# Optimization experiments

Measured on AMD Instinct MI355X. Metric: run time of the kernel, lower is better.

## Reference

```python
import jax, jax.numpy as jnp
import numpy as np

N_NODES = 20000
DEG = 16
T_IN = 12
T_OUT = 24
N_HEADS = 4
N_CH = 4
BATCH = 2


def setup_inputs() -> dict:
    key = jax.random.key(0)
    k1, k2, k3, k4 = jax.random.split(key, 4)
    # unique directed edges: (i, (i+d) % N) for d in 1..DEG, plus self loops
    src = jnp.repeat(jnp.arange(N_NODES, dtype=jnp.int64), DEG)
    offs = jnp.tile(jnp.arange(1, DEG + 1, dtype=jnp.int64), N_NODES)
    dst = (src + offs) % N_NODES
    loops = jnp.arange(N_NODES, dtype=jnp.int64)
    d_edges = jnp.concatenate([
        jnp.stack([src, dst], axis=1),
        jnp.stack([loops, loops], axis=1),
    ], axis=0)  # (E, 2), E = N*DEG + N
    E = d_edges.shape[0]
    x = jax.random.normal(k1, (BATCH, T_IN, N_NODES, N_CH), dtype=jnp.float32)
    d_ew = jax.random.uniform(k2, (E, N_HEADS), dtype=jnp.float32)
    # shrink: Linear(t_in*n_heads -> T-t_in)
    fan_in = T_IN * N_HEADS
    bound = 1.0 / np.sqrt(fan_in)
    W = jax.random.uniform(k3, (T_OUT - T_IN, fan_in), minval=-bound, maxval=bound, dtype=jnp.float32)
    b = jax.random.uniform(k4, (T_OUT - T_IN,), minval=-bound, maxval=bound, dtype=jnp.float32)
    return {"x": x, "d_ew": d_ew, "W": W, "b": b, "d_edges": d_edges}


def reference(x, d_ew, W, b, d_edges):
    # x: (B, t, N, C); d_ew: (E, H); d_edges: (E, 2)
    node_i = d_edges[:, 0]
    node_j = d_edges[:, 1]
    B, t, N, C = x.shape
    # gather source node features per edge -> (E, B, t, C)
    x_src = jnp.moveaxis(x[:, :, node_i, :], 2, 0)
    # messages: (E, B, t, H, C)
    msg = d_ew[:, None, None, :, None] * x_src[:, :, :, None, :]
    # scatter-add into destination nodes (equivalent to the dense N x N holder sum)
    agg = jax.ops.segment_sum(msg, node_j, num_segments=N)  # (N, B, t, H, C)
    y = jnp.moveaxis(agg, 0, 2)                              # (B, t, N, H, C)
    # permute(0,2,4,1,3) -> (B, N, C, t, H), flatten (t, H)
    y = jnp.transpose(y, (0, 2, 4, 1, 3)).reshape(B, N, C, t * d_ew.shape[1])
    y = jax.nn.relu(jnp.einsum('bncf,of->bnco', y, W) + b)   # (B, N, C, T-t)
    y = jnp.transpose(y, (0, 3, 1, 2))                       # (B, T-t, N, C)
    return jnp.concatenate([x, y], axis=1)                   # (B, T, N, C)
```

## Files before the change

kernel.cpp:

```cpp
#include <hip/hip_runtime.h>

namespace {
constexpr int NN  = 20000;
constexpr int DEG = 16;
constexpr int TI  = 12;
constexpr int TO  = 24;
constexpr int NC  = 4;
constexpr int NB  = 2;
constexpr int ESELF  = NN * DEG;
constexpr int TILE   = 32;
constexpr int NTILES = NN / TILE;
constexpr int WN     = TILE + 16;
constexpr int EWP    = 68;
}

__global__ __launch_bounds__(256) void gnn_fused(
    const float* __restrict__ x,
    const float* __restrict__ ew,
    const float* __restrict__ W,
    const float* __restrict__ bias,
    float* __restrict__ out)
{
    __shared__ float x_lds[TI * WN * NC];
    __shared__ float ew_lds[WN * EWP];
    __shared__ float ews[TILE * 4];
    __shared__ float red[TILE * NC][13];

    const int tid = threadIdx.x;
    const int bid = blockIdx.x;
    const int b   = bid / NTILES;
    const int n0  = (bid % NTILES) * TILE;

    const float4* ew4 = reinterpret_cast<const float4*>(ew);

#pragma unroll
    for (int i = 0; i < 3; ++i) {
        const int idx = tid + 256 * i;
        const int sl  = idx >> 4;
        const int r4  = idx & 15;
        int s = n0 - 16 + sl;
        s += (s >> 31) & NN;
        const float4 v = ew4[s * DEG + r4];
        *reinterpret_cast<float4*>(&ew_lds[sl * EWP + r4 * 4]) = v;
    }
    if (tid < TILE) {
        const float4 v = ew4[ESELF + n0 + tid];
        *reinterpret_cast<float4*>(&ews[tid * 4]) = v;
    }
    {
        const size_t xb = (size_t)b * TI * NN * NC;
#pragma unroll
        for (int i = 0; i < 9; ++i) {
            const int f = tid + 256 * i;
            const int t = f / (WN * NC);
            const int r = f - t * (WN * NC);
            int s = n0 - 16 + (r >> 2);
            s += (s >> 31) & NN;
            x_lds[f] = x[xb + (size_t)t * NN * NC + s * NC + (r & 3)];
        }
    }
    __syncthreads();

    const int tg = tid >> 7;
    const int nl = (tid >> 2) & 31;
    const int c  = tid & 3;
    const int t0 = __builtin_amdgcn_readfirstlane(tg * 6);

    float agg[6][4] = {{0.f}};

#pragma unroll
    for (int k = 0; k < DEG; ++k) {
        const int wi = nl + 15 - k;
        const float4 w = *reinterpret_cast<const float4*>(&ew_lds[wi * EWP + 4 * k]);
#pragma unroll
        for (int j = 0; j < 6; ++j) {
            const float xv = x_lds[(t0 + j) * (WN * NC) + wi * 4 + c];
            agg[j][0] = fmaf(w.x, xv, agg[j][0]);
            agg[j][1] = fmaf(w.y, xv, agg[j][1]);
            agg[j][2] = fmaf(w.z, xv, agg[j][2]);
            agg[j][3] = fmaf(w.w, xv, agg[j][3]);
        }
    }

    const size_t obase = (size_t)b * TO * NN * NC + (n0 + nl) * NC + c;

    {
        const float4 w = *reinterpret_cast<const float4*>(&ews[nl * 4]);
        const int wi = nl + 16;
#pragma unroll
        for (int j = 0; j < 6; ++j) {
            const float xv = x_lds[(t0 + j) * (WN * NC) + wi * 4 + c];
            out[obase + (size_t)(t0 + j) * NN * NC] = xv;
            agg[j][0] = fmaf(w.x, xv, agg[j][0]);
            agg[j][1] = fmaf(w.y, xv, agg[j][1]);
            agg[j][2] = fmaf(w.z, xv, agg[j][2]);
            agg[j][3] = fmaf(w.w, xv, agg[j][3]);
        }
    }

    float y[12];
#pragma unroll
    for (int o = 0; o < 12; ++o) {
        float acc = 0.f;
#pragma unroll
        for (int j = 0; j < 6; ++j)
#pragma unroll
            for (int h = 0; h < 4; ++h)
                acc = fmaf(W[o * 48 + (t0 + j) * 4 + h], agg[j][h], acc);
        y[o] = acc;
    }

    if (tg == 1) {
#pragma unroll
        for (int o = 0; o < 12; ++o) red[nl * 4 + c][o] = y[o];
    }
    __syncthreads();
    if (tg == 0) {
#pragma unroll
        for (int o = 0; o < 12; ++o) {
            const float v = fmaxf(y[o] + red[nl * 4 + c][o] + bias[o], 0.f);
            out[obase + (size_t)(TI + o) * NN * NC] = v;
        }
    }
}

extern "C" void kernel_launch(void* const* d_in, const int* in_sizes, int n_in,
                              void* d_out, int out_size, void* d_ws, size_t ws_size,
                              hipStream_t stream) {
    const float* x    = (const float*)d_in[0];
    const float* ew   = (const float*)d_in[1];
    const float* W    = (const float*)d_in[2];
    const float* bias = (const float*)d_in[3];
    float* out = (float*)d_out;

    const int blocks = NB * NTILES;
    hipLaunchKernelGGL(gnn_fused, dim3(blocks), dim3(256), 0, stream,
                       x, ew, W, bias, out);
}
```

Measured before the change: 16.98 us.

## Use packed FMA with two channels per thread and async global-to-LDS loads

Halves the block to 128 threads, with each thread handling two channels as float2 and updating them through v_pk_fma_f32 inline asm with op_sel broadcasts. The x tile is loaded by __builtin_amdgcn_global_load_lds, 16 bytes per lane, instead of per-float register staging. Outputs and the reduction buffer move to float2 stores. This aims to cut FMA issue count and load instructions, but it doubles per-thread register use and relies on correct handling of the LDS-direct layout and wait semantics.

```diff
diff --git a/kernel.cpp b/kernel.cpp
--- a/kernel.cpp
+++ b/kernel.cpp
@@ -4,122 +4,150 @@
 constexpr int NN  = 20000;
 constexpr int DEG = 16;
 constexpr int TI  = 12;
-constexpr int TO  = 24;
-constexpr int NC  = 4;
 constexpr int NB  = 2;
 constexpr int ESELF  = NN * DEG;
 constexpr int TILE   = 32;
 constexpr int NTILES = NN / TILE;
-constexpr int WN     = TILE + 16;
+constexpr int WN     = 48;
 constexpr int EWP    = 68;
+constexpr int REDP   = 13;
 }
 
-__global__ __launch_bounds__(256) void gnn_fused(
+__device__ __forceinline__ void pk_fma(float2& d, float2 a, float2 b) {
+    asm("v_pk_fma_f32 %0, %1, %2, %0" : "+v"(d) : "v"(a), "v"(b));
+}
+__device__ __forceinline__ void pk_fma_blo(float2& d, float2 a, float2 b) {
+    asm("v_pk_fma_f32 %0, %1, %2, %0 op_sel:[0,0,0] op_sel_hi:[1,0,1]"
+        : "+v"(d) : "v"(a), "v"(b));
+}
+__device__ __forceinline__ void pk_fma_bhi(float2& d, float2 a, float2 b) {
+    asm("v_pk_fma_f32 %0, %1, %2, %0 op_sel:[0,1,0] op_sel_hi:[1,1,1]"
+        : "+v"(d) : "v"(a), "v"(b));
+}
+
+__global__ __launch_bounds__(128) void gnn_fused(
     const float* __restrict__ x,
     const float* __restrict__ ew,
     const float* __restrict__ W,
     const float* __restrict__ bias,
     float* __restrict__ out)
 {
-    __shared__ float x_lds[TI * WN * NC];
+    __shared__ float x_lds[TI * WN * 4];
     __shared__ float ew_lds[WN * EWP];
     __shared__ float ews[TILE * 4];
-    __shared__ float red[TILE * NC][13];
+    __shared__ float red[TILE * 2 * REDP * 2];
 
     const int tid = threadIdx.x;
     const int bid = blockIdx.x;
     const int b   = bid / NTILES;
     const int n0  = (bid % NTILES) * TILE;
 
-    const float4* ew4 = reinterpret_cast<const float4*>(ew);
-
+    {
+        const float* xb = x + (size_t)b * TI * NN * 4;
 #pragma unroll
-    for (int i = 0; i < 3; ++i) {
-        const int idx = tid + 256 * i;
-        const int sl  = idx >> 4;
-        const int r4  = idx & 15;
-        int s = n0 - 16 + sl;
-        s += (s >> 31) & NN;
-        const float4 v = ew4[s * DEG + r4];
-        *reinterpret_cast<float4*>(&ew_lds[sl * EWP + r4 * 4]) = v;
-    }
-    if (tid < TILE) {
-        const float4 v = ew4[ESELF + n0 + tid];
-        *reinterpret_cast<float4*>(&ews[tid * 4]) = v;
+        for (int i = 0; i < 5; ++i) {
+            if (i < 4 || tid < 64) {
+                const int idx4 = tid + 128 * i;
+                const int t  = idx4 / WN;
+                const int wi = idx4 - t * WN;
+                int s = n0 - 16 + wi; s += (s >> 31) & NN;
+                const float* src = xb + (size_t)(t * NN + s) * 4;
+                float* dstbase = x_lds + (size_t)(128 * i + (tid & 64)) * 4;
+                __builtin_amdgcn_global_load_lds(
+                    (const __attribute__((address_space(1))) void*)src,
+                    (__attribute__((address_space(3))) void*)dstbase, 16, 0, 0);
+            }
+        }
     }
     {
-        const size_t xb = (size_t)b * TI * NN * NC;
+        const float4* ew4 = (const float4*)ew;
 #pragma unroll
-        for (int i = 0; i < 9; ++i) {
-            const int f = tid + 256 * i;
-            const int t = f / (WN * NC);
-            const int r = f - t * (WN * NC);
-            int s = n0 - 16 + (r >> 2);
-            s += (s >> 31) & NN;
-            x_lds[f] = x[xb + (size_t)t * NN * NC + s * NC + (r & 3)];
+        for (int i = 0; i < 6; ++i) {
+            const int idx = tid + 128 * i;
+            const int sl = idx >> 4, r4 = idx & 15;
+            int s = n0 - 16 + sl; s += (s >> 31) & NN;
+            const float4 v = ew4[s * DEG + r4];
+            *(float4*)&ew_lds[sl * EWP + r4 * 4] = v;
         }
+        if (tid < TILE) ((float4*)ews)[tid] = ew4[ESELF + n0 + tid];
     }
     __syncthreads();
 
-    const int tg = tid >> 7;
-    const int nl = (tid >> 2) & 31;
-    const int c  = tid & 3;
+    const int c2 = tid & 1;
+    const int nl = (tid >> 1) & 31;
+    const int tg = tid >> 6;
     const int t0 = __builtin_amdgcn_readfirstlane(tg * 6);
 
-    float agg[6][4] = {{0.f}};
+    float2 agg[6][4] = {};
 
 #pragma unroll
     for (int k = 0; k < DEG; ++k) {
         const int wi = nl + 15 - k;
-        const float4 w = *reinterpret_cast<const float4*>(&ew_lds[wi * EWP + 4 * k]);
+        const float4 e4 = *(const float4*)&ew_lds[wi * EWP + 4 * k];
+        const float2 e01 = {e4.x, e4.y}, e23 = {e4.z, e4.w};
 #pragma unroll
         for (int j = 0; j < 6; ++j) {
-            const float xv = x_lds[(t0 + j) * (WN * NC) + wi * 4 + c];
-            agg[j][0] = fmaf(w.x, xv, agg[j][0]);
-            agg[j][1] = fmaf(w.y, xv, agg[j][1]);
-            agg[j][2] = fmaf(w.z, xv, agg[j][2]);
-            agg[j][3] = fmaf(w.w, xv, agg[j][3]);
+            const float2 xv =
+                *(const float2*)&x_lds[(t0 + j) * (WN * 4) + wi * 4 + c2 * 2];
+            pk_fma_blo(agg[j][0], xv, e01);
+            pk_fma_bhi(agg[j][1], xv, e01);
+            pk_fma_blo(agg[j][2], xv, e23);
+            pk_fma_bhi(agg[j][3], xv, e23);
         }
     }
 
-    const size_t obase = (size_t)b * TO * NN * NC + (n0 + nl) * NC + c;
-
     {
-        const float4 w = *reinterpret_cast<const float4*>(&ews[nl * 4]);
-        const int wi = nl + 16;
+        const size_t ob = (size_t)b * 24 * NN * 4 + (size_t)(n0 + nl) * 4 + c2 * 2;
+        const float2 e01 = *(const float2*)&ews[nl * 4 + 0];
+        const float2 e23 = *(const float2*)&ews[nl * 4 + 2];
 #pragma unroll
         for (int j = 0; j < 6; ++j) {
-            const float xv = x_lds[(t0 + j) * (WN * NC) + wi * 4 + c];
-            out[obase + (size_t)(t0 + j) * NN * NC] = xv;
-            agg[j][0] = fmaf(w.x, xv, agg[j][0]);
-            agg[j][1] = fmaf(w.y, xv, agg[j][1]);
-            agg[j][2] = fmaf(w.z, xv, agg[j][2]);
-            agg[j][3] = fmaf(w.w, xv, agg[j][3]);
+            const float2 xv =
+                *(const float2*)&x_lds[(t0 + j) * (WN * 4) + (nl + 16) * 4 + c2 * 2];
+            *(float2*)&out[ob + (size_t)(t0 + j) * NN * 4] = xv;
+            pk_fma_blo(agg[j][0], xv, e01);
+            pk_fma_bhi(agg[j][1], xv, e01);
+            pk_fma_blo(agg[j][2], xv, e23);
+            pk_fma_bhi(agg[j][3], xv, e23);
         }
     }
 
-    float y[12];
+    float2 y2[12];
 #pragma unroll
     for (int o = 0; o < 12; ++o) {
-        float acc = 0.f;
+        float2 acc = {0.f, 0.f};
 #pragma unroll
-        for (int j = 0; j < 6; ++j)
-#pragma unroll
-            for (int h = 0; h < 4; ++h)
-                acc = fmaf(W[o * 48 + (t0 + j) * 4 + h], agg[j][h], acc);
-        y[o] = acc;
+        for (int j = 0; j < 6; ++j) {
+            const float* Wr = W + o * 48 + (t0 + j) * 4;
+            acc.x = fmaf(Wr[0], agg[j][0].x, acc.x);
+            acc.y = fmaf(Wr[0], agg[j][0].y, acc.y);
+            acc.x = fmaf(Wr[1], agg[j][1].x, acc.x);
+            acc.y = fmaf(Wr[1], agg[j][1].y, acc.y);
+            acc.x = fmaf(Wr[2], agg[j][2].x, acc.x);
+            acc.y = fmaf(Wr[2], agg[j][2].y, acc.y);
+            acc.x = fmaf(Wr[3], agg[j][3].x, acc.x);
+            acc.y = fmaf(Wr[3], agg[j][3].y, acc.y);
+        }
+        y2[o] = acc;
     }
 
     if (tg == 1) {
+        float* r = red + (size_t)(nl * 2 + c2) * REDP * 2;
 #pragma unroll
-        for (int o = 0; o < 12; ++o) red[nl * 4 + c][o] = y[o];
+        for (int o = 0; o < 12; ++o) *(float2*)&r[o * 2] = y2[o];
     }
     __syncthreads();
     if (tg == 0) {
+        const float* r = red + (size_t)(nl * 2 + c2) * REDP * 2;
+        const size_t ob = (size_t)(b * 24 + 12) * NN * 4
+                        + (size_t)(n0 + nl) * 4 + c2 * 2;
 #pragma unroll
         for (int o = 0; o < 12; ++o) {
-            const float v = fmaxf(y[o] + red[nl * 4 + c][o] + bias[o], 0.f);
-            out[obase + (size_t)(TI + o) * NN * NC] = v;
+            const float2 p = *(const float2*)&r[o * 2];
+            const float bo = bias[o];
+            float2 v = {fmaxf(y2[o].x + p.x + bo, 0.f),
+                        fmaxf(y2[o].y + p.y + bo, 0.f)};
+            *(float2*)&out[ob + (size_t)o * NN * 4] = v;
         }
     }
 }
@@ -134,6 +162,6 @@
     float* out = (float*)d_out;
 
     const int blocks = NB * NTILES;
-    hipLaunchKernelGGL(gnn_fused, dim3(blocks), dim3(256), 0, stream,
+    hipLaunchKernelGGL(gnn_fused, dim3(blocks), dim3(128), 0, stream,
                        x, ew, W, bias, out);
 }
```

Result: no change. 17.00 us (+0.1%).
